# Kernel optimization log

Hardware: AMD Instinct MI355X
Metric: run time of the kernel (lower is better)

## Reference

```python
import jax, jax.numpy as jnp
import numpy as np

B, DIM, N = 2, 1024, 2048
HEADS, DHEAD = 16, 64
INNER = HEADS * DHEAD
THETA, SCALE_BASE = 10000.0, 8192.0


def setup_inputs() -> dict:
    key = jax.random.key(0)
    k1, k2, k3, k4 = jax.random.split(key, 4)
    x = jax.random.normal(k1, (B, DIM, N), dtype=jnp.float32)
    # Conv1d kernel-size-1 weights are plain matrices
    w_qkv = jax.random.normal(k2, (3 * INNER, DIM), dtype=jnp.float32) * (DIM ** -0.5)
    w_out = jax.random.normal(k3, (DIM, INNER), dtype=jnp.float32) * (INNER ** -0.5)
    b_out = jax.random.normal(k4, (DIM,), dtype=jnp.float32) * 0.02
    return {"x": x, "w_qkv": w_qkv, "w_out": w_out, "b_out": b_out}


def _rope_cos_sin(n, dtype):
    # inv_freq: [DHEAD/2]; t scaled so max position ~ scale_base
    inv_freq = 1.0 / (THETA ** (jnp.arange(0, DHEAD, 2, dtype=jnp.float32) / DHEAD))
    t = jnp.arange(n, dtype=jnp.float32) * (SCALE_BASE / n)
    freqs = inv_freq[:, None] * t[None, :]          # [DHEAD/2, n]
    emb = jnp.concatenate([freqs, freqs], axis=0)   # [DHEAD, n]
    return jnp.cos(emb).astype(dtype), jnp.sin(emb).astype(dtype)


def _rotate_half(t):
    # t: [b, h, d, n]; split along d
    t1, t2 = jnp.split(t, 2, axis=2)
    return jnp.concatenate([-t2, t1], axis=2)


def reference(x, w_qkv, w_out, b_out):
    b, _, n = x.shape
    # QKV projection (Conv1d k=1, no bias): [b, 3*inner, n]
    qkv = jnp.einsum('od,bdn->bon', w_qkv, x)
    q, k, v = jnp.split(qkv, 3, axis=1)
    # b (h d) n -> b h d n
    q, k, v = (t.reshape(b, HEADS, DHEAD, n) for t in (q, k, v))
    # rotary embedding
    cos, sin = _rope_cos_sin(n, x.dtype)            # [DHEAD, n]
    cos, sin = cos[None, None], sin[None, None]
    q = q * cos + _rotate_half(q) * sin
    k = k * cos + _rotate_half(k) * sin
    # manual attention; scale = q.shape[-2]**-0.5 = DHEAD**-0.5
    scale = DHEAD ** -0.5
    sim = jnp.einsum('bhdi,bhdj->bhij', q * scale, k)
    attn = jax.nn.softmax(sim, axis=-1)
    out = jnp.einsum('bhij,bhdj->bhdi', attn, v)    # [b, h, d, n]
    out = out.reshape(b, INNER, n)
    # output projection (Conv1d k=1, with bias)
    return jnp.einsum('oi,bin->bon', w_out, out) + b_out[None, :, None]
```

## Files before the change

kernel.cpp:

```cpp
#include <hip/hip_runtime.h>
#include <stdint.h>

#define BATCH 2
#define DIM 1024
#define NSEQ 2048
#define HEADS 16
#define DHEAD 64
#define INNER 1024
#define O3 3072

typedef __attribute__((ext_vector_type(8))) short bf16x8;
typedef __attribute__((ext_vector_type(4))) float f32x4;

__device__ __forceinline__ short f2bf(float f) {
  unsigned int u = __builtin_bit_cast(unsigned int, f);
  unsigned int r = (u + 0x7fffu + ((u >> 16) & 1u)) >> 16;
  return (short)(unsigned short)r;
}
__device__ __forceinline__ float bf2f(short s) {
  unsigned int u = ((unsigned int)(unsigned short)s) << 16;
  return __builtin_bit_cast(float, u);
}

__global__ void k_cast_weights(const float* __restrict__ wq, const float* __restrict__ wo,
                               short* __restrict__ wq_bf, short* __restrict__ wo_bf) {
  int i = blockIdx.x * 256 + threadIdx.x;
  const int NQ4 = O3 * DIM / 4;
  const float4* src;
  unsigned int* dst;
  int j;
  if (i < NQ4) { src = (const float4*)wq; dst = (unsigned int*)wq_bf; j = i; }
  else         { src = (const float4*)wo; dst = (unsigned int*)wo_bf; j = i - NQ4; }
  float4 v = src[j];
  unsigned int lo = ((unsigned int)(unsigned short)f2bf(v.y) << 16) | (unsigned short)f2bf(v.x);
  unsigned int hi = ((unsigned int)(unsigned short)f2bf(v.w) << 16) | (unsigned short)f2bf(v.z);
  dst[j * 2] = lo;
  dst[j * 2 + 1] = hi;
}

__global__ void k_rope_table(float* __restrict__ tab) {
  int i = blockIdx.x * 256 + threadIdx.x;
  int n = i >> 5, d = i & 31;
  float inv = powf(10000.0f, -(float)d * (1.0f / 32.0f));
  float ang = inv * (4.0f * (float)n);
  float s, c;
  sincosf(ang, &s, &c);
  tab[n * 64 + d] = c;
  tab[n * 64 + 32 + d] = s;
}

__global__ void k_transpose_x(const float* __restrict__ x, short* __restrict__ xt) {
  __shared__ short tile[64 * 65];
  int nt = blockIdx.x, dt = blockIdx.y, b = blockIdx.z;
  int t = threadIdx.x;
  int tc = t & 63, tr = t >> 6;
  const float* xp = x + ((size_t)b * DIM + dt * 64) * NSEQ + nt * 64;
  #pragma unroll
  for (int r = 0; r < 16; ++r) {
    int d = r * 4 + tr;
    tile[d * 65 + tc] = f2bf(xp[(size_t)d * NSEQ + tc]);
  }
  __syncthreads();
  short* op = xt + ((size_t)b * NSEQ + nt * 64) * DIM + dt * 64;
  #pragma unroll
  for (int r = 0; r < 16; ++r) {
    int n = r * 4 + tr;
    op[(size_t)n * DIM + tc] = tile[tc * 65 + n];
  }
}

template <int EPI>
__global__ __launch_bounds__(256) void k_gemm(const short* __restrict__ A,
                                              const short* __restrict__ Bmat,
                                              short* __restrict__ Cbf, float* __restrict__ Cf,
                                              const float* __restrict__ bias, int M, int K) {
  __shared__ __align__(16) short lds_a[128 * 32];
  __shared__ __align__(16) short lds_b[128 * 32];
  const int t = threadIdx.x;
  const int lane = t & 63, w = t >> 6;
  const int lr = lane & 15, lg = lane >> 4;
  const int m0 = blockIdx.y * 128, n0 = blockIdx.x * 128;
  const int wm = (w >> 1) * 64, wn = (w & 1) * 64;

  const short* Bp = Bmat + (size_t)blockIdx.z * NSEQ * K;

  const int srow = t >> 2, sslot = t & 3;
  const short* ga0 = A + (size_t)(m0 + srow) * K + sslot * 8;
  const short* ga1 = ga0 + (size_t)64 * K;
  const short* gb0 = Bp + (size_t)(n0 + srow) * K + sslot * 8;
  const short* gb1 = gb0 + (size_t)64 * K;
  const int sa0 = srow * 32 + ((sslot ^ ((srow >> 1) & 3)) << 3);

  f32x4 acc[4][4];
  const f32x4 zf = {0.f, 0.f, 0.f, 0.f};
  #pragma unroll
  for (int i = 0; i < 4; ++i)
    #pragma unroll
    for (int j = 0; j < 4; ++j) acc[i][j] = zf;

  bf16x8 ra0 = *(const bf16x8*)ga0, ra1 = *(const bf16x8*)ga1;
  bf16x8 rb0 = *(const bf16x8*)gb0, rb1 = *(const bf16x8*)gb1;

  const int nkt = K >> 5;
  for (int kt = 0; kt < nkt; ++kt) {
    __syncthreads();
    *(bf16x8*)&lds_a[sa0] = ra0; *(bf16x8*)&lds_a[sa0 + 2048] = ra1;
    *(bf16x8*)&lds_b[sa0] = rb0; *(bf16x8*)&lds_b[sa0 + 2048] = rb1;
    __syncthreads();
    if (kt + 1 < nkt) {
      ga0 += 32; ga1 += 32; gb0 += 32; gb1 += 32;
      ra0 = *(const bf16x8*)ga0; ra1 = *(const bf16x8*)ga1;
      rb0 = *(const bf16x8*)gb0; rb1 = *(const bf16x8*)gb1;
    }
    bf16x8 af[4], bfr[4];
    #pragma unroll
    for (int mi = 0; mi < 4; ++mi) {
      int row = wm + mi * 16 + lr;
      af[mi] = *(const bf16x8*)&lds_a[row * 32 + ((lg ^ ((row >> 1) & 3)) << 3)];
    }
    #pragma unroll
    for (int nj = 0; nj < 4; ++nj) {
      int row = wn + nj * 16 + lr;
      bfr[nj] = *(const bf16x8*)&lds_b[row * 32 + ((lg ^ ((row >> 1) & 3)) << 3)];
    }
    #pragma unroll
    for (int mi = 0; mi < 4; ++mi)
      #pragma unroll
      for (int nj = 0; nj < 4; ++nj)
        acc[mi][nj] = __builtin_amdgcn_mfma_f32_16x16x32_bf16(af[mi], bfr[nj], acc[mi][nj], 0, 0, 0);
  }

  if (EPI == 0) {
    short* Cp = Cbf + (size_t)blockIdx.z * M * NSEQ;
    #pragma unroll
    for (int mi = 0; mi < 4; ++mi)
      #pragma unroll
      for (int nj = 0; nj < 4; ++nj)
        #pragma unroll
        for (int r = 0; r < 4; ++r) {
          int row = m0 + wm + mi * 16 + lg * 4 + r;
          int col = n0 + wn + nj * 16 + lr;
          Cp[(size_t)row * NSEQ + col] = f2bf(acc[mi][nj][r]);
        }
  } else {
    float* Cp = Cf + (size_t)blockIdx.z * M * NSEQ;
    #pragma unroll
    for (int mi = 0; mi < 4; ++mi)
      #pragma unroll
      for (int nj = 0; nj < 4; ++nj)
        #pragma unroll
        for (int r = 0; r < 4; ++r) {
          int row = m0 + wm + mi * 16 + lg * 4 + r;
          int col = n0 + wn + nj * 16 + lr;
          Cp[(size_t)row * NSEQ + col] = acc[mi][nj][r] + bias[row];
        }
  }
}

__global__ void k_ropeK(const short* __restrict__ qkv, const float* __restrict__ tab,
                        short* __restrict__ Kt) {
  __shared__ short lt[64 * 64];
  const int t = threadIdx.x;
  const int nc = blockIdx.x, h = blockIdx.y, b = blockIdx.z;
  const short* src = qkv + ((size_t)(b * O3 + INNER + h * 64)) * NSEQ + nc * 64;
  {
    int dl = t >> 2, q4 = t & 3;
    #pragma unroll
    for (int v = 0; v < 2; ++v) {
      bf16x8 x = *(const bf16x8*)(src + (size_t)dl * NSEQ + q4 * 16 + v * 8);
      #pragma unroll
      for (int e = 0; e < 8; ++e) {
        int n = q4 * 16 + v * 8 + e;
        lt[n * 64 + (dl ^ ((n & 7) << 3))] = x[e];
      }
    }
  }
  __syncthreads();
  const int dseg = t & 7;
  #pragma unroll
  for (int itn = 0; itn < 2; ++itn) {
    int n = (t >> 3) + itn * 32;
    int gn = nc * 64 + n;
    bf16x8 v0 = *(const bf16x8*)&lt[n * 64 + ((dseg ^ (n & 7)) << 3)];
    bf16x8 vp = *(const bf16x8*)&lt[n * 64 + (((dseg ^ 4) ^ (n & 7)) << 3)];
    const float* tb = tab + (size_t)gn * 64 + (dseg & 3) * 8;
    float sgn = (dseg < 4) ? -1.0f : 1.0f;
    bf16x8 outv;
    #pragma unroll
    for (int e = 0; e < 8; ++e) {
      float c = tb[e], s = tb[32 + e];
      outv[e] = f2bf(bf2f(v0[e]) * c + sgn * bf2f(vp[e]) * s);
    }
    *(bf16x8*)(Kt + (((size_t)(b * HEADS + h)) * NSEQ + gn) * 64 + dseg * 8) = outv;
  }
}

__global__ __launch_bounds__(256) void k_attn(const short* __restrict__ qkv,
                                              const short* __restrict__ Kt,
                                              const float* __restrict__ tab,
                                              short* __restrict__ AOt) {
  __shared__ __align__(16) short smem[16384];
  const int t = threadIdx.x, lane = t & 63, w = t >> 6;
  const int lr = lane & 15, lg = lane >> 4;
  const int L = ((blockIdx.x & 7) << 6) | (blockIdx.x >> 3);
  const int it = L & 15, h = (L >> 4) & 15, b = L >> 8;
  const int i0 = it * 128;

  const short* Qsrc = qkv + ((size_t)(b * O3 + h * 64)) * NSEQ;
  {
    int dl = t >> 2, q4 = t & 3;
    const short* gq = Qsrc + (size_t)dl * NSEQ + i0 + q4 * 32;
    #pragma unroll
    for (int kk = 0; kk < 4; ++kk) {
      bf16x8 x = *(const bf16x8*)(gq + kk * 8);
      *(bf16x8*)&smem[dl * 128 + (((q4 * 4 + kk) ^ (dl & 7)) << 3)] = x;
    }
  }
  __syncthreads();
  bf16x8 aq[2][2];
  #pragma unroll
  for (int sub = 0; sub < 2; ++sub) {
    int il = w * 32 + sub * 16 + lr;
    int gn = i0 + il;
    float q0[8], q1[8];
    #pragma unroll
    for (int e = 0; e < 8; ++e) {
      int d0 = lg * 8 + e;
      int sw = (((il >> 3) ^ e) << 3) + (il & 7);
      q0[e] = bf2f(smem[d0 * 128 + sw]);
      q1[e] = bf2f(smem[(d0 + 32) * 128 + sw]);
    }
    const float* tb = tab + (size_t)gn * 64 + lg * 8;
    bf16x8 a0, a1;
    #pragma unroll
    for (int e = 0; e < 8; ++e) {
      float c = tb[e], s = tb[32 + e];
      a0[e] = f2bf((q0[e] * c - q1[e] * s) * 0.125f);
      a1[e] = f2bf((q1[e] * c + q0[e] * s) * 0.125f);
    }
    aq[sub][0] = a0; aq[sub][1] = a1;
  }

  const short* Kh = Kt + ((size_t)(b * HEADS + h)) * NSEQ * 64;
  const short* Vh = qkv + ((size_t)(b * O3 + 2 * INNER + h * 64)) * NSEQ;
  short* lds_k = smem;
  short* lds_v = smem + 4096;
  short* lds_p = smem + 8192 + w * 2048;

  f32x4 o_acc[2][4];
  f32x4 sum_acc[2];
  const f32x4 zf = {0.f, 0.f, 0.f, 0.f};
  const f32x4 c10 = {-10.f, -10.f, -10.f, -10.f};
  #pragma unroll
  for (int sub = 0; sub < 2; ++sub) {
    sum_acc[sub] = zf;
    #pragma unroll
    for (int dg = 0; dg < 4; ++dg) o_acc[sub][dg] = zf;
  }
  bf16x8 ones;
  #pragma unroll
  for (int e = 0; e < 8; ++e) ones[e] = (short)0x3F80;

  const int srow = t >> 3, sslot = t & 7;
  const short* gk0 = Kh + (size_t)srow * 64 + sslot * 8;
  const short* gk1 = gk0 + 32 * 64;
  const short* gv0 = Vh + (size_t)srow * NSEQ + sslot * 8;
  const short* gv1 = gv0 + (size_t)32 * NSEQ;
  const int sk0 = srow * 64 + ((sslot ^ (srow & 7)) << 3);

  bf16x8 rk0 = *(const bf16x8*)gk0, rk1 = *(const bf16x8*)gk1;
  bf16x8 rv0 = *(const bf16x8*)gv0, rv1 = *(const bf16x8*)gv1;

  for (int jt = 0; jt < NSEQ / 64; ++jt) {
    __syncthreads();
    *(bf16x8*)&lds_k[sk0] = rk0; *(bf16x8*)&lds_k[sk0 + 2048] = rk1;
    *(bf16x8*)&lds_v[sk0] = rv0; *(bf16x8*)&lds_v[sk0 + 2048] = rv1;
    __syncthreads();
    if (jt + 1 < NSEQ / 64) {
      gk0 += 64 * 64; gk1 += 64 * 64; gv0 += 64; gv1 += 64;
      rk0 = *(const bf16x8*)gk0; rk1 = *(const bf16x8*)gk1;
      rv0 = *(const bf16x8*)gv0; rv1 = *(const bf16x8*)gv1;
    }
    f32x4 sA[4], sB[4];
    __builtin_amdgcn_s_setprio(1);
    #pragma unroll
    for (int jg = 0; jg < 4; ++jg) {
      int row = jg * 16 + lr;
      bf16x8 bk0 = *(const bf16x8*)&lds_k[row * 64 + ((lg ^ (row & 7)) << 3)];
      bf16x8 bk1 = *(const bf16x8*)&lds_k[row * 64 + (((4 + lg) ^ (row & 7)) << 3)];
      sA[jg] = __builtin_amdgcn_mfma_f32_16x16x32_bf16(aq[0][0], bk0, c10, 0, 0, 0);
      sA[jg] = __builtin_amdgcn_mfma_f32_16x16x32_bf16(aq[0][1], bk1, sA[jg], 0, 0, 0);
      sB[jg] = __builtin_amdgcn_mfma_f32_16x16x32_bf16(aq[1][0], bk0, c10, 0, 0, 0);
      sB[jg] = __builtin_amdgcn_mfma_f32_16x16x32_bf16(aq[1][1], bk1, sB[jg], 0, 0, 0);
    }
    __builtin_amdgcn_s_setprio(0);
    bf16x8 bv[2][4];
    #pragma unroll
    for (int sub = 0; sub < 2; ++sub) {
      short* pb = lds_p + sub * 1024;
      #pragma unroll
      for (int jg = 0; jg < 4; ++jg)
        #pragma unroll
        for (int r = 0; r < 4; ++r) {
          float p = __expf(sub ? sB[jg][r] : sA[jg][r]);
          int ir = 4 * lg + r;
          pb[ir * 64 + (((jg * 2 + (lr >> 3)) ^ (ir & 7)) << 3) + (lr & 7)] = f2bf(p);
        }
      #pragma unroll
      for (int jj = 0; jj < 2; ++jj) {
        bf16x8 ap = *(const bf16x8*)&pb[lr * 64 + (((jj * 4 + lg) ^ (lr & 7)) << 3)];
        sum_acc[sub] = __builtin_amdgcn_mfma_f32_16x16x32_bf16(ones, ap, sum_acc[sub], 0, 0, 0);
        if (sub == 0) {
          #pragma unroll
          for (int dg = 0; dg < 4; ++dg) {
            int row = dg * 16 + lr;
            bv[jj][dg] = *(const bf16x8*)&lds_v[row * 64 + (((jj * 4 + lg) ^ (row & 7)) << 3)];
          }
        }
        __builtin_amdgcn_s_setprio(1);
        #pragma unroll
        for (int dg = 0; dg < 4; ++dg)
          o_acc[sub][dg] = __builtin_amdgcn_mfma_f32_16x16x32_bf16(ap, bv[jj][dg], o_acc[sub][dg], 0, 0, 0);
        __builtin_amdgcn_s_setprio(0);
      }
    }
  }
  short* Op = AOt + (size_t)b * NSEQ * INNER;
  #pragma unroll
  for (int sub = 0; sub < 2; ++sub) {
    float l0 = sum_acc[sub][0];
    float inv[4];
    #pragma unroll
    for (int r = 0; r < 4; ++r) inv[r] = 1.0f / __shfl(l0, 4 * lg + r, 64);
    #pragma unroll
    for (int dg = 0; dg < 4; ++dg)
      #pragma unroll
      for (int r = 0; r < 4; ++r) {
        int n = i0 + w * 32 + sub * 16 + 4 * lg + r;
        int c = h * 64 + dg * 16 + lr;
        Op[(size_t)n * INNER + c] = f2bf(o_acc[sub][dg][r] * inv[r]);
      }
  }
}

extern "C" void kernel_launch(void* const* d_in, const int* in_sizes, int n_in,
                              void* d_out, int out_size, void* d_ws, size_t ws_size,
                              hipStream_t stream) {
  const float* x = (const float*)d_in[0];
  const float* w_qkv = (const float*)d_in[1];
  const float* w_out = (const float*)d_in[2];
  const float* b_out = (const float*)d_in[3];
  float* out = (float*)d_out;
  char* ws = (char*)d_ws;
  short* wq_bf = (short*)(ws + 0);
  short* wo_bf = (short*)(ws + 6291456);
  short* Xt    = (short*)(ws + 8388608);
  float* tab   = (float*)(ws + 16777216);
  short* qkv   = (short*)(ws + 17301504);
  short* Kt    = (short*)(ws + 42467328);
  short* AOt   = (short*)(ws + 50855936);

  k_cast_weights<<<4096, 256, 0, stream>>>(w_qkv, w_out, wq_bf, wo_bf);
  k_rope_table<<<256, 256, 0, stream>>>(tab);
  k_transpose_x<<<dim3(32, 16, BATCH), 256, 0, stream>>>(x, Xt);
  k_gemm<0><<<dim3(16, 24, BATCH), 256, 0, stream>>>(wq_bf, Xt, qkv, nullptr, nullptr, O3, DIM);
  k_ropeK<<<dim3(32, 16, BATCH), 256, 0, stream>>>(qkv, tab, Kt);
  k_attn<<<512, 256, 0, stream>>>(qkv, Kt, tab, AOt);
  k_gemm<1><<<dim3(16, 8, BATCH), 256, 0, stream>>>(wo_bf, AOt, nullptr, out, b_out, INNER, INNER);
}
```

Before: 197.6 us.

## Double-buffer GEMM LDS via direct global-to-LDS loads with XCD block swizzle

Rewrites the bf16 GEMM main loop to use global_load_lds to stream tiles straight into a double-buffered LDS, prefetching the next K-tile while MFMAs run on the current one. It drops the register staging and the XOR bank swizzle, and raises wave priority around the MFMA block. The grid becomes 1D with a remapping that groups blocks by XCD. The aim is to hide load latency and cut a barrier per iteration, at the cost of doubled LDS use and possible bank conflicts from the unswizzled layout.

Result: slower. 203.4 us (+2.9%).

```diff
diff --git a/kernel.cpp b/kernel.cpp
--- a/kernel.cpp
+++ b/kernel.cpp
@@ -12,6 +12,9 @@
 typedef __attribute__((ext_vector_type(8))) short bf16x8;
 typedef __attribute__((ext_vector_type(4))) float f32x4;
 
+typedef __attribute__((address_space(3))) unsigned int* as3u;
+typedef const __attribute__((address_space(1))) unsigned int* as1u;
+
 __device__ __forceinline__ short f2bf(float f) {
   unsigned int u = __builtin_bit_cast(unsigned int, f);
   unsigned int r = (u + 0x7fffu + ((u >> 16) & 1u)) >> 16;
@@ -20,6 +23,9 @@
 __device__ __forceinline__ float bf2f(short s) {
   unsigned int u = ((unsigned int)(unsigned short)s) << 16;
   return __builtin_bit_cast(float, u);
+}
+__device__ __forceinline__ void gload16(const short* g, short* l) {
+  __builtin_amdgcn_global_load_lds((as1u)(const void*)g, (as3u)(void*)l, 16, 0, 0);
 }
 
 __global__ void k_cast_weights(const float* __restrict__ wq, const float* __restrict__ wo,
@@ -74,22 +80,32 @@
                                               const short* __restrict__ Bmat,
                                               short* __restrict__ Cbf, float* __restrict__ Cf,
                                               const float* __restrict__ bias, int M, int K) {
-  __shared__ __align__(16) short lds_a[128 * 32];
-  __shared__ __align__(16) short lds_b[128 * 32];
+  __shared__ __align__(16) short lds_a[2][128 * 32];
+  __shared__ __align__(16) short lds_b[2][128 * 32];
   const int t = threadIdx.x;
   const int lane = t & 63, w = t >> 6;
   const int lr = lane & 15, lg = lane >> 4;
-  const int m0 = blockIdx.y * 128, n0 = blockIdx.x * 128;
+  const int cpx = gridDim.x >> 3;
+  const int swz = (blockIdx.x & 7) * cpx + (blockIdx.x >> 3);
+  const int mtiles = M >> 7;
+  const int n0 = (swz & 15) * 128;
+  const int rest = swz >> 4;
+  const int m0 = (rest % mtiles) * 128;
+  const int bz = rest / mtiles;
+
+  const short* Bp = Bmat + (size_t)bz * NSEQ * K;
+  const short* gA = A + (size_t)(m0 + 32 * w + (lane >> 2)) * K + (lane & 3) * 8;
+  const short* gB = Bp + (size_t)(n0 + 32 * w + (lane >> 2)) * K + (lane & 3) * 8;
   const int wm = (w >> 1) * 64, wn = (w & 1) * 64;
 
-  const short* Bp = Bmat + (size_t)blockIdx.z * NSEQ * K;
-
-  const int srow = t >> 2, sslot = t & 3;
-  const short* ga0 = A + (size_t)(m0 + srow) * K + sslot * 8;
-  const short* ga1 = ga0 + (size_t)64 * K;
-  const short* gb0 = Bp + (size_t)(n0 + srow) * K + sslot * 8;
-  const short* gb1 = gb0 + (size_t)64 * K;
-  const int sa0 = srow * 32 + ((sslot ^ ((srow >> 1) & 3)) << 3);
+  auto STAGE = [&](int buf, int kk) {
+    const short* ga = gA + kk * 32;
+    const short* gb = gB + kk * 32;
+    gload16(ga, &lds_a[buf][(32 * w) * 32]);
+    gload16(ga + (size_t)16 * K, &lds_a[buf][(32 * w + 16) * 32]);
+    gload16(gb, &lds_b[buf][(32 * w) * 32]);
+    gload16(gb + (size_t)16 * K, &lds_b[buf][(32 * w + 16) * 32]);
+  };
 
   f32x4 acc[4][4];
   const f32x4 zf = {0.f, 0.f, 0.f, 0.f};
@@ -98,40 +114,35 @@
     #pragma unroll
     for (int j = 0; j < 4; ++j) acc[i][j] = zf;
 
-  bf16x8 ra0 = *(const bf16x8*)ga0, ra1 = *(const bf16x8*)ga1;
-  bf16x8 rb0 = *(const bf16x8*)gb0, rb1 = *(const bf16x8*)gb1;
+  STAGE(0, 0);
+  asm volatile("s_waitcnt vmcnt(0)" ::: "memory");
+  __syncthreads();
 
   const int nkt = K >> 5;
+  int cur = 0;
   for (int kt = 0; kt < nkt; ++kt) {
-    __syncthreads();
-    *(bf16x8*)&lds_a[sa0] = ra0; *(bf16x8*)&lds_a[sa0 + 2048] = ra1;
-    *(bf16x8*)&lds_b[sa0] = rb0; *(bf16x8*)&lds_b[sa0 + 2048] = rb1;
-    __syncthreads();
-    if (kt + 1 < nkt) {
-      ga0 += 32; ga1 += 32; gb0 += 32; gb1 += 32;
-      ra0 = *(const bf16x8*)ga0; ra1 = *(const bf16x8*)ga1;
-      rb0 = *(const bf16x8*)gb0; rb1 = *(const bf16x8*)gb1;
-    }
+    if (kt + 1 < nkt) STAGE(cur ^ 1, kt + 1);
     bf16x8 af[4], bfr[4];
     #pragma unroll
-    for (int mi = 0; mi < 4; ++mi) {
-      int row = wm + mi * 16 + lr;
-      af[mi] = *(const bf16x8*)&lds_a[row * 32 + ((lg ^ ((row >> 1) & 3)) << 3)];
-    }
-    #pragma unroll
-    for (int nj = 0; nj < 4; ++nj) {
-      int row = wn + nj * 16 + lr;
-      bfr[nj] = *(const bf16x8*)&lds_b[row * 32 + ((lg ^ ((row >> 1) & 3)) << 3)];
-    }
+    for (int mi = 0; mi < 4; ++mi)
+      af[mi] = *(const bf16x8*)&lds_a[cur][(wm + mi * 16 + lr) * 32 + lg * 8];
+    #pragma unroll
+    for (int nj = 0; nj < 4; ++nj)
+      bfr[nj] = *(const bf16x8*)&lds_b[cur][(wn + nj * 16 + lr) * 32 + lg * 8];
+    __builtin_amdgcn_s_setprio(1);
     #pragma unroll
     for (int mi = 0; mi < 4; ++mi)
       #pragma unroll
       for (int nj = 0; nj < 4; ++nj)
         acc[mi][nj] = __builtin_amdgcn_mfma_f32_16x16x32_bf16(af[mi], bfr[nj], acc[mi][nj], 0, 0, 0);
+    __builtin_amdgcn_s_setprio(0);
+    asm volatile("s_waitcnt vmcnt(0)" ::: "memory");
+    __syncthreads();
+    cur ^= 1;
   }
 
   if (EPI == 0) {
-    short* Cp = Cbf + (size_t)blockIdx.z * M * NSEQ;
+    short* Cp = Cbf + (size_t)bz * M * NSEQ;
     #pragma unroll
     for (int mi = 0; mi < 4; ++mi)
       #pragma unroll
@@ -143,7 +154,7 @@
           Cp[(size_t)row * NSEQ + col] = f2bf(acc[mi][nj][r]);
         }
   } else {
-    float* Cp = Cf + (size_t)blockIdx.z * M * NSEQ;
+    float* Cp = Cf + (size_t)bz * M * NSEQ;
     #pragma unroll
     for (int mi = 0; mi < 4; ++mi)
       #pragma unroll
@@ -363,8 +374,8 @@
   k_cast_weights<<<4096, 256, 0, stream>>>(w_qkv, w_out, wq_bf, wo_bf);
   k_rope_table<<<256, 256, 0, stream>>>(tab);
   k_transpose_x<<<dim3(32, 16, BATCH), 256, 0, stream>>>(x, Xt);
-  k_gemm<0><<<dim3(16, 24, BATCH), 256, 0, stream>>>(wq_bf, Xt, qkv, nullptr, nullptr, O3, DIM);
+  k_gemm<0><<<768, 256, 0, stream>>>(wq_bf, Xt, qkv, nullptr, nullptr, O3, DIM);
   k_ropeK<<<dim3(32, 16, BATCH), 256, 0, stream>>>(qkv, tab, Kt);
   k_attn<<<512, 256, 0, stream>>>(qkv, Kt, tab, AOt);
-  k_gemm<1><<<dim3(16, 8, BATCH), 256, 0, stream>>>(wo_bf, AOt, nullptr, out, b_out, INNER, INNER);
-}
+  k_gemm<1><<<256, 256, 0, stream>>>(wo_bf, AOt, nullptr, out, b_out, INNER, INNER);
+}
```
